# Kernel tuning notes

Hardware: AMD Instinct MI355X
Metric: run time of the kernel (lower is better)

The kernel has to match this reference:

```python
import jax, jax.numpy as jnp
import numpy as np

# ---- static config (matches module defaults / init_kwargs) ----
SX = 256; SY = 256; C = 3; NK = 12; B = 4
R = 10; DT = 0.2; DD = 5; SIGMA = 0.65; THETA_A = 1.0; N_EXP = 2


def _build_kernels():
    """Replicates compute_kernel(): multi-ring Lenia kernels, normalized in real space."""
    rng = np.random.default_rng(42)
    mid = SX // 2
    g = np.mgrid[-mid:mid, -mid:mid]
    dist = np.linalg.norm(g, axis=0)  # [SX, SY]
    Ks = []
    for _ in range(NK):
        r = rng.uniform(0.3, 1.0)
        a = rng.uniform(0.0, 1.0, 3)
        w = rng.uniform(0.05, 0.2, 3)
        b = rng.uniform(0.0, 1.0, 3)
        D = dist / ((R + 15) * r)
        sig = 1.0 / (1.0 + np.exp((D - 1.0) * 10.0))  # sigmoid(-(D-1)*10)
        kerf = (b[None, None, :] * np.exp(-(((D[..., None] - a[None, None, :]) / w[None, None, :]) ** 2) / 2.0)).sum(-1)
        Ks.append(sig * kerf)
    K = np.stack(Ks, axis=-1)  # [SX, SY, NK]
    Kn = K / K.sum(axis=(0, 1), keepdims=True)
    m = rng.uniform(0.05, 0.5, NK)
    s = rng.uniform(0.01, 0.18, NK)
    h = rng.uniform(0.2, 1.0, NK)
    return (Kn.astype(np.float32), m.astype(np.float32), s.astype(np.float32), h.astype(np.float32))


def setup_inputs() -> dict:
    key = jax.random.key(0)
    Kn, m, s, h = _build_kernels()
    A = jax.random.uniform(key, (B, 1, SX, SY, C), dtype=jnp.float32)
    c0 = jnp.asarray(np.arange(NK) % C, dtype=jnp.int32)      # source channel of each kernel
    c1_map = jnp.asarray(np.arange(NK) % C, dtype=jnp.int32)  # target channel of each kernel
    return {"A": A, "Kn": jnp.asarray(Kn), "m": jnp.asarray(m), "s": jnp.asarray(s),
            "h": jnp.asarray(h), "c0": c0, "c1_map": c1_map}


def _sobel(A):
    """Circular (torus) Sobel, separable [1,2,1]x[-1,0,1]/8, on spatial axes (2,3).
    A: [B,1,SX,SY,C] -> [B,1,SX,SY,2,C] (d/dx, d/dy)."""
    sy = jnp.roll(A, -1, 3) + 2.0 * A + jnp.roll(A, 1, 3)
    gx = (jnp.roll(sy, -1, 2) - jnp.roll(sy, 1, 2)) / 8.0
    sx = jnp.roll(A, -1, 2) + 2.0 * A + jnp.roll(A, 1, 2)
    gy = (jnp.roll(sx, -1, 3) - jnp.roll(sx, 1, 3)) / 8.0
    return jnp.stack([gx, gy], axis=4)


def _forward(A, Kn, m, s, h, c0, c1_map):
    # FFT-domain convolution per kernel
    fK = jnp.fft.fft2(jnp.fft.fftshift(Kn, axes=(0, 1)), axes=(0, 1))  # [SX,SY,NK] complex
    fA = jnp.fft.fft2(A, axes=(2, 3))                                   # [B,1,SX,SY,C]
    fAk = fA[..., c0]                                                    # [B,1,SX,SY,NK]
    U = jnp.fft.ifft2(fK[None, None] * fAk, axes=(2, 3)).real           # [B,1,SX,SY,NK]
    # growth(U,m,s) = 2*bell(U,m,s)-1, scaled by h
    G = (2.0 * jnp.exp(-((U - m) ** 2) / (2.0 * s ** 2)) - 1.0) * h
    # sum kernel contributions into their target channel (c1)
    M = jax.nn.one_hot(c1_map, C, dtype=G.dtype)                         # [NK,C]
    Uc = jnp.einsum('bzxyk,kc->bzxyc', G, M)                             # [B,1,SX,SY,C]
    nabla_U = _sobel(Uc)                                                 # [B,1,SX,SY,2,C]
    nabla_A = _sobel(A.sum(-1, keepdims=True))                           # [B,1,SX,SY,2,1]
    alpha = jnp.clip((A[:, :, :, :, None, :] / THETA_A) ** N_EXP, 0.0, 1.0)
    F = nabla_U * (1.0 - alpha) - nabla_A * alpha                        # flow field
    # ---- reintegration tracking (RT) over a (2*DD+1)^2 neighborhood ----
    x = jnp.arange(SX, dtype=F.dtype); y = jnp.arange(SY, dtype=F.dtype)
    pos = jnp.stack(jnp.meshgrid(x, y, indexing='ij'), axis=-1) + 0.5    # [SX,SY,2]
    ma = DD - SIGMA
    mus = pos[None, None, :, :, :, None] + jnp.clip(DT * F, -ma, ma)     # target centers [B,1,SX,SY,2,C]
    offsets = jnp.asarray([(dx, dy) for dx in range(-DD, DD + 1) for dy in range(-DD, DD + 1)], dtype=jnp.int32)
    amax = min(1.0, 2.0 * SIGMA)

    def body(acc, off):
        dx, dy = off[0], off[1]
        rollA = jnp.roll(A, (dx, dy), axis=(2, 3))
        rollmu = jnp.roll(mus, (dx, dy), axis=(2, 3))
        dpmu = jnp.abs(pos[None, None, :, :, :, None] - rollmu)
        sz = 0.5 - dpmu + SIGMA
        area = jnp.prod(jnp.clip(sz, 0.0, amax), axis=4) / (4.0 * SIGMA ** 2)  # [B,1,SX,SY,C]
        return acc + rollA * area, None

    nA, _ = jax.lax.scan(jax.checkpoint(body), jnp.zeros_like(A), offsets)
    return nA


def reference(A, Kn, m, s, h, c0, c1_map):
    return _forward(A, Kn, m, s, h, c0, c1_map)
```

## Files before the change

kernel.cpp:

```cpp
#include <hip/hip_runtime.h>


typedef _Float16 f16;
typedef __attribute__((ext_vector_type(8))) _Float16 half8;
typedef __attribute__((ext_vector_type(16))) float f32x16;

#define RMAX 44
#define NROWS 89
#define NDMAX 8
#define NFRAG (3*NROWS*NDMAX)
#define ST 168
#define TROWS 120
#define SCHED_STRIDE 1024
#define KTHR 1e-7f

__global__ __launch_bounds__(128) void lenia_meta(const float* __restrict__ Kn,
                                                  int2* __restrict__ meta,
                                                  int* __restrict__ rowr) {
    int blk = blockIdx.x;
    int c = blk / NROWS, ri = blk - c * NROWS;
    int di = ri - RMAX;
    int t = threadIdx.x;
    int dj = t - RMAX;
    int act = 0;
    if (t < NROWS) {
        size_t base = (size_t)(((di + 128) << 8) | (dj + 128)) * 12 + c;
        float k0 = Kn[base], k1 = Kn[base + 3], k2 = Kn[base + 6], k3 = Kn[base + 9];
        act = (fmaxf(fmaxf(k0, k1), fmaxf(k2, k3)) > KTHR) ? 1 : 0;
    }
    __shared__ int smn[128], smx[128];
    smn[t] = act ? dj : 1000;
    smx[t] = act ? dj : -1000;
    __syncthreads();
    for (int s = 64; s > 0; s >>= 1) {
        if (t < s) { smn[t] = min(smn[t], smn[t + s]); smx[t] = max(smx[t], smx[t + s]); }
        __syncthreads();
    }
    if (t == 0) {
        int jmn = smn[0], jmx = smx[0];
        if (jmx < jmn) { meta[blk] = make_int2(1, 0); rowr[blk] = 0; }
        else {
            meta[blk] = make_int2(jmn, jmx);
            rowr[blk] = max(abs(di), max(abs(jmn), abs(jmx)));
        }
    }
}

__global__ __launch_bounds__(128) void lenia_sched(const int2* __restrict__ meta,
                                                   const int* __restrict__ rowr,
                                                   int2* __restrict__ meta2,
                                                   unsigned int* __restrict__ sched,
                                                   int* __restrict__ nsched,
                                                   int* __restrict__ radii) {
    int c = blockIdx.x;
    int t = threadIdx.x;
    __shared__ int pre[NROWS], nds[NROWS], rmx[128];
    int nd = 0, d0 = 0;
    if (t < NROWS) {
        int2 bm = meta[c * NROWS + t];
        if (bm.y >= bm.x) {
            d0 = ((bm.x - 7) >> 3) << 3;
            nd = ((bm.y + 7 - d0) >> 4) + 1;
        }
        meta2[c * NROWS + t] = make_int2(d0, nd);
        nds[t] = nd;
    }
    rmx[t] = (t < NROWS) ? rowr[c * NROWS + t] : 0;
    __syncthreads();
    for (int s = 64; s > 0; s >>= 1) {
        if (t < s) rmx[t] = max(rmx[t], rmx[t + s]);
        __syncthreads();
    }
    __shared__ int tot;
    if (t == 0) {
        radii[c] = rmx[0];
        int acc = 0;
        for (int i = 0; i < NROWS; ++i) { pre[i] = acc; acc += nds[i]; }
        tot = acc;
    }
    __syncthreads();
    if (t < NROWS && nd > 0) {
        int base = pre[t];
        for (int i = 0; i < nd; ++i) {
            int delta = d0 + 16 * i;
            unsigned int off = (unsigned int)(t * ST + delta + 128);
            sched[c * SCHED_STRIDE + base + i] =
                (unsigned int)((c * NROWS + t) * NDMAX + i) | (off << 12);
        }
    }
    if (t == 0) {
        int ns = (tot + 7) & ~7;
        unsigned int padoff = (unsigned int)(RMAX * ST + 128);
        for (int i = tot; i < ns + 48; ++i)
            sched[c * SCHED_STRIDE + i] = (unsigned int)NFRAG | (padoff << 12);
        nsched[c] = ns;
    }
}

__global__ __launch_bounds__(256) void lenia_trans(const float* __restrict__ Kn,
                                                   const float* __restrict__ A,
                                                   f16* __restrict__ Ktr,
                                                   f16* __restrict__ Atr) {
    int blk = blockIdx.x, tid = threadIdx.x;
    if (blk < 256) {
        int gid = blk * 256 + tid;
        const float4* kp = (const float4*)(Kn + (size_t)gid * 12);
        float4 v0 = kp[0], v1 = kp[1], v2 = kp[2];
        Ktr[0 * 65536 + gid]  = (f16)v0.x;  Ktr[1 * 65536 + gid]  = (f16)v0.y;
        Ktr[2 * 65536 + gid]  = (f16)v0.z;  Ktr[3 * 65536 + gid]  = (f16)v0.w;
        Ktr[4 * 65536 + gid]  = (f16)v1.x;  Ktr[5 * 65536 + gid]  = (f16)v1.y;
        Ktr[6 * 65536 + gid]  = (f16)v1.z;  Ktr[7 * 65536 + gid]  = (f16)v1.w;
        Ktr[8 * 65536 + gid]  = (f16)v2.x;  Ktr[9 * 65536 + gid]  = (f16)v2.y;
        Ktr[10 * 65536 + gid] = (f16)v2.z;  Ktr[11 * 65536 + gid] = (f16)v2.w;
    } else {
        int px = (blk - 256) * 256 + tid;
        int b = px >> 16, rem = px & 65535;
        const float* ap = A + (size_t)px * 3;
        Atr[(size_t)(b * 3 + 0) * 65536 + rem] = (f16)ap[0];
        Atr[(size_t)(b * 3 + 1) * 65536 + rem] = (f16)ap[1];
        Atr[(size_t)(b * 3 + 2) * 65536 + rem] = (f16)ap[2];
    }
}

__global__ __launch_bounds__(256) void lenia_bpack(const f16* __restrict__ Ktr,
                                                   const int2* __restrict__ meta2,
                                                   uint4* __restrict__ bpack) {
    int fi = blockIdx.x * 4 + (threadIdx.x >> 6);
    int l = threadIdx.x & 63;
    if (fi > NFRAG) return;
    union { f16 h[8]; uint4 u; } pk;
    if (fi == NFRAG) {
        pk.u = make_uint4(0, 0, 0, 0);
        bpack[(size_t)fi * 64 + l] = pk.u;
        return;
    }
    int c = fi / (NROWS * NDMAX);
    int rem = fi - c * (NROWS * NDMAX);
    int ri = rem >> 3, didx = rem & 7;
    int di = ri - RMAX;
    int delta = meta2[c * NROWS + ri].x + 16 * didx;
    int q = (l & 31) >> 3, sy = l & 7, g = l >> 5;
    int dj0 = delta + 8 * g - sy;
    const f16* src = Ktr + (size_t)(c + 3 * q) * 65536 + ((di + 128) << 8) + (dj0 + 128);
    #pragma unroll
    for (int j = 0; j < 8; ++j) pk.h[j] = src[j];
    bpack[(size_t)fi * 64 + l] = pk.u;
}

__global__ __launch_bounds__(256) void lenia_conv(
        const f16* __restrict__ Atr, const uint4* __restrict__ bpack,
        const unsigned int* __restrict__ sched, const int* __restrict__ nsched,
        const int* __restrict__ radii,
        const float* __restrict__ mp, const float* __restrict__ sp,
        const float* __restrict__ hp, f16* __restrict__ Uc) {
    extern __shared__ f16 smh[];

    const int tid = threadIdx.x;
    const int bc = blockIdx.y;
    const int b = bc / 3, c = bc - b * 3;
    const int x0 = (blockIdx.x >> 3) << 5;
    const int y0 = (blockIdx.x & 7) << 5;

    const int R = __builtin_amdgcn_readfirstlane(min(max(radii[c], 1), RMAX));
    const int R8 = (R + 7) & ~7;
    const int colbase = y0 - R8 - 16;
    const int rows = 32 + 2 * R;
    const f16* Ap = Atr + (size_t)(b * 3 + c) * 65536;

    {
        int nchunk = rows * 21;
        int tr = tid / 21, rem = tid - tr * 21;
        for (int ci = tid; ci < nchunk; ci += 256) {
            int gi = (x0 - R + tr) & 255;
            int gj = (colbase + rem * 8) & 255;
            *(half8*)(smh + tr * ST + rem * 8) = *(const half8*)(Ap + (gi << 8) + gj);
            tr += 12; rem += 4;
            if (rem >= 21) { rem -= 21; ++tr; }
        }
    }
    __syncthreads();

    const int lane = tid & 63, wid = tid >> 6;
    const int m = lane & 31, g = lane >> 5;
    const int abase = (m + R - RMAX) * ST + 8 * wid + R8 + 16 + 8 * g - 128;

    const unsigned int* sW = sched + c * SCHED_STRIDE;
    const int ns = __builtin_amdgcn_readfirstlane(nsched[c]);

    f32x16 accE, accO;
    #pragma unroll
    for (int r = 0; r < 16; ++r) { accE[r] = 0.f; accO[r] = 0.f; }

    unsigned int eq[16];
    uint4 bq[16];
    #pragma unroll
    for (int j = 0; j < 16; ++j) {
        eq[j] = sW[j];
        bq[j] = bpack[(size_t)(eq[j] & 4095u) * 64 + lane];
    }

    for (int it = 0; it < ns; it += 16) {
        #pragma unroll
        for (int j = 0; j < 16; j += 2) {
            {
                half8 av = *(const half8*)(smh + abase + (int)(eq[j] >> 12));
                union { uint4 u; half8 h; } bb; bb.u = bq[j];
                accE = __builtin_amdgcn_mfma_f32_32x32x16_f16(av, bb.h, accE, 0, 0, 0);
                unsigned int ne = sW[it + 16 + j];
                eq[j] = ne;
                bq[j] = bpack[(size_t)(ne & 4095u) * 64 + lane];
            }
            {
                half8 av = *(const half8*)(smh + abase + (int)(eq[j + 1] >> 12));
                union { uint4 u; half8 h; } bb; bb.u = bq[j + 1];
                accO = __builtin_amdgcn_mfma_f32_32x32x16_f16(av, bb.h, accO, 0, 0, 0);
                unsigned int ne = sW[it + 17 + j];
                eq[j + 1] = ne;
                bq[j + 1] = bpack[(size_t)(ne & 4095u) * 64 + lane];
            }
        }
    }

    const int q = (lane & 31) >> 3, sy = lane & 7;
    const float mq = mp[c + 3 * q];
    const float sq = sp[c + 3 * q];
    const float hq = hp[c + 3 * q];
    const float i2s = 1.f / (2.f * sq * sq);
    #pragma unroll
    for (int r = 0; r < 16; ++r) {
        float d = (accE[r] + accO[r]) - mq;
        float gg = (2.f * expf(-d * d * i2s) - 1.f) * hq;
        gg += __shfl_xor(gg, 8);
        gg += __shfl_xor(gg, 16);
        if ((lane & 24) == 0) {
            int row = (r & 3) + ((r >> 2) << 3) + (g << 2);
            Uc[((size_t)(b << 16) + ((x0 + row) << 8) + (y0 + 8 * wid + sy)) * 3 + c] = (f16)gg;
        }
    }
}

#define FTW 44
#define FSW 45
#define PLH (FSW * FTW)
__global__ __launch_bounds__(256) void lenia_flowrt(
        const f16* __restrict__ Atr, const f16* __restrict__ Uc,
        float* __restrict__ out) {
    extern __shared__ char fraw[];
    f16*    ucp = (f16*)fraw;
    f16*    atp = (f16*)(fraw + PLH * 2);
    float2* muq = (float2*)(fraw + 8 * PLH);

    int bc = blockIdx.y;
    int b = bc / 3, c = bc - b * 3;
    int t = blockIdx.x;
    int x0 = (t >> 3) << 5, y0 = (t & 7) << 5;
    const f16* A0 = Atr + (size_t)(b * 3) * 65536;
    const f16* Ub = Uc + ((size_t)b << 16) * 3;

    for (int idx = threadIdx.x; idx < FTW * FTW; idx += 256) {
        int si = idx / FTW, sj = idx - si * FTW;
        int gi = (x0 - 6 + si) & 255, gj = (y0 - 6 + sj) & 255;
        int pix = (gi << 8) + gj;
        int o = si * FSW + sj;
        ucp[o] = Ub[(size_t)pix * 3 + c];
        atp[o] = A0[pix];
        atp[PLH + o] = A0[65536 + pix];
        atp[2 * PLH + o] = A0[131072 + pix];
    }
    __syncthreads();

    for (int idx = threadIdx.x; idx < 42 * 42; idx += 256) {
        int ci = idx / 42, cj = idx - ci * 42;
        int si = ci + 1, sj = cj + 1;
        int o = si * FSW + sj;
        int vx = x0 - 6 + si, vy = y0 - 6 + sj;
        float sx = (vx < 0 || vx > 255) ? 1e7f : 0.f;
        float syv = (vy < 0 || vy > 255) ? 1e7f : 0.f;

        float as[3][3];
        #pragma unroll
        for (int i = 0; i < 3; ++i)
            #pragma unroll
            for (int j = 0; j < 3; ++j) {
                int oo = o + (i - 1) * FSW + (j - 1);
                as[i][j] = (float)atp[oo] + (float)atp[PLH + oo] + (float)atp[2 * PLH + oo];
            }
        float gxA = ((as[2][0] + 2.f * as[2][1] + as[2][2])
                   - (as[0][0] + 2.f * as[0][1] + as[0][2])) * 0.125f;
        float gyA = ((as[0][2] + 2.f * as[1][2] + as[2][2])
                   - (as[0][0] + 2.f * as[1][0] + as[2][0])) * 0.125f;

        float u00 = ucp[o - FSW - 1], u01 = ucp[o - FSW], u02 = ucp[o - FSW + 1];
        float u10 = ucp[o - 1],                          u12 = ucp[o + 1];
        float u20 = ucp[o + FSW - 1], u21 = ucp[o + FSW], u22 = ucp[o + FSW + 1];
        float gx = ((u20 + 2.f * u21 + u22) - (u00 + 2.f * u01 + u02)) * 0.125f;
        float gy = ((u02 + 2.f * u12 + u22) - (u00 + 2.f * u10 + u20)) * 0.125f;
        float a = (float)atp[c * PLH + o];
        float alpha = fminf(a * a, 1.f);
        float Fx = gx * (1.f - alpha) - gxA * alpha;
        float Fy = gy * (1.f - alpha) - gyA * alpha;
        float dx = fminf(fmaxf(0.2f * Fx, -4.35f), 4.35f) + sx;
        float dy = fminf(fmaxf(0.2f * Fy, -4.35f), 4.35f) + syv;
        muq[o] = make_float2(dx, dy);
    }
    __syncthreads();

    int tx = threadIdx.x & 31, tyg = threadIdx.x >> 5;
    int ty0 = tyg << 2;
    float a0 = 0.f, a1 = 0.f, a2 = 0.f, a3 = 0.f;
    const f16* ac = atp + c * PLH;

    for (int dxs = 0; dxs < 11; ++dxs) {
        float fdx = (float)(5 - dxs);
        int rowb = (tx + 1 + dxs) * FSW + (ty0 + 1);
        #pragma unroll
        for (int sjj = 0; sjj < 14; ++sjj) {
            float fdy = (float)(5 - sjj);
            float2 mu = muq[rowb + sjj];
            float av = (float)ac[rowb + sjj];
            float wx = fminf(fmaxf(1.15f - fabsf(fdx - mu.x), 0.f), 1.f);
            float awx = av * wx;
            float e0 = fdy - mu.y;
            a0 = fmaf(awx, fminf(fmaxf(1.15f - fabsf(e0), 0.f), 1.f), a0);
            a1 = fmaf(awx, fminf(fmaxf(1.15f - fabsf(e0 + 1.f), 0.f), 1.f), a1);
            a2 = fmaf(awx, fminf(fmaxf(1.15f - fabsf(e0 + 2.f), 0.f), 1.f), a2);
            a3 = fmaf(awx, fminf(fmaxf(1.15f - fabsf(e0 + 3.f), 0.f), 1.f), a3);
        }
    }
    const float inv = 1.0f / 1.69f;
    size_t ob = ((size_t)(b << 16) + ((x0 + tx) << 8) + (y0 + ty0)) * 3 + c;
    out[ob]     = a0 * inv;
    out[ob + 3] = a1 * inv;
    out[ob + 6] = a2 * inv;
    out[ob + 9] = a3 * inv;
}

extern "C" void kernel_launch(void* const* d_in, const int* in_sizes, int n_in,
                              void* d_out, int out_size, void* d_ws, size_t ws_size,
                              hipStream_t stream) {
    const float* A  = (const float*)d_in[0];
    const float* Kn = (const float*)d_in[1];
    const float* m  = (const float*)d_in[2];
    const float* s  = (const float*)d_in[3];
    const float* h  = (const float*)d_in[4];

    char* ws = (char*)d_ws;
    int*          radii = (int*)ws;
    int*          nschd = (int*)(ws + 16);
    int*          rowr  = (int*)(ws + 64);
    int2*         meta  = (int2*)(ws + 2048);
    int2*         meta2 = (int2*)(ws + 8192);
    unsigned int* sched = (unsigned int*)(ws + 16384);
    f16*          Ktr   = (f16*)(ws + 32768);
    f16*          Atr   = (f16*)(ws + 1605632);
    uint4*        bpack = (uint4*)(ws + 3178496);
    f16*          Uc    = (f16*)(ws + 32768);

    lenia_meta<<<3 * NROWS, 128, 0, stream>>>(Kn, meta, rowr);
    lenia_sched<<<3, 128, 0, stream>>>(meta, rowr, meta2, sched, nschd, radii);
    lenia_trans<<<1280, 256, 0, stream>>>(Kn, A, Ktr, Atr);
    lenia_bpack<<<(NFRAG + 4) / 4, 256, 0, stream>>>(Ktr, meta2, bpack);
    lenia_conv<<<dim3(64, 12), 256, TROWS * ST * sizeof(f16), stream>>>(
        Atr, bpack, sched, nschd, radii, m, s, h, Uc);
    lenia_flowrt<<<dim3(64, 12), 256, 8 * PLH + PLH * 8, stream>>>(
        Atr, Uc, (float*)d_out);
}
```

Measured before the change: 74.95 us.

## Fuse kernel transpose into bpack and scalarize schedule loads in conv

Removes the separate Ktr fp16 transpose of the full kernel tensor and builds the MFMA B-fragments straight from Kn inside a merged prep kernel that also converts A. This drops one launch and a full write and read of the 1.5 MB transposed kernel buffer, at the cost of strided 12-float reads from Kn when packing. The conv loop also wraps schedule entries in readfirstlane so the offsets stay uniform scalars, which can cut VGPR use and vector address math. The workspace layout is reassigned so Uc no longer aliases the removed Ktr region.

```diff
diff --git a/kernel.cpp b/kernel.cpp
--- a/kernel.cpp
+++ b/kernel.cpp
@@ -9,6 +9,7 @@
 #define NROWS 89
 #define NDMAX 8
 #define NFRAG (3*NROWS*NDMAX)
+#define NBPK ((NFRAG + 4) / 4)
 #define ST 168
 #define TROWS 120
 #define SCHED_STRIDE 1024
@@ -97,54 +98,41 @@
     }
 }
 
-__global__ __launch_bounds__(256) void lenia_trans(const float* __restrict__ Kn,
+__global__ __launch_bounds__(256) void lenia_prep2(const float* __restrict__ Kn,
                                                    const float* __restrict__ A,
-                                                   f16* __restrict__ Ktr,
+                                                   const int2* __restrict__ meta2,
+                                                   uint4* __restrict__ bpack,
                                                    f16* __restrict__ Atr) {
-    int blk = blockIdx.x, tid = threadIdx.x;
-    if (blk < 256) {
-        int gid = blk * 256 + tid;
-        const float4* kp = (const float4*)(Kn + (size_t)gid * 12);
-        float4 v0 = kp[0], v1 = kp[1], v2 = kp[2];
-        Ktr[0 * 65536 + gid]  = (f16)v0.x;  Ktr[1 * 65536 + gid]  = (f16)v0.y;
-        Ktr[2 * 65536 + gid]  = (f16)v0.z;  Ktr[3 * 65536 + gid]  = (f16)v0.w;
-        Ktr[4 * 65536 + gid]  = (f16)v1.x;  Ktr[5 * 65536 + gid]  = (f16)v1.y;
-        Ktr[6 * 65536 + gid]  = (f16)v1.z;  Ktr[7 * 65536 + gid]  = (f16)v1.w;
-        Ktr[8 * 65536 + gid]  = (f16)v2.x;  Ktr[9 * 65536 + gid]  = (f16)v2.y;
-        Ktr[10 * 65536 + gid] = (f16)v2.z;  Ktr[11 * 65536 + gid] = (f16)v2.w;
+    int blk = blockIdx.x;
+    if (blk < NBPK) {
+        int fi = blk * 4 + (threadIdx.x >> 6);
+        int l = threadIdx.x & 63;
+        if (fi > NFRAG) return;
+        union { f16 h[8]; uint4 u; } pk;
+        if (fi == NFRAG) {
+            pk.u = make_uint4(0, 0, 0, 0);
+            bpack[(size_t)fi * 64 + l] = pk.u;
+            return;
+        }
+        int c = fi / (NROWS * NDMAX);
+        int rem = fi - c * (NROWS * NDMAX);
+        int ri = rem >> 3, didx = rem & 7;
+        int di = ri - RMAX;
+        int delta = meta2[c * NROWS + ri].x + 16 * didx;
+        int q = (l & 31) >> 3, sy = l & 7, g = l >> 5;
+        int dj0 = delta + 8 * g - sy;
+        const float* src = Kn + (size_t)(((di + 128) << 8) + (dj0 + 128)) * 12 + c + 3 * q;
+        #pragma unroll
+        for (int j = 0; j < 8; ++j) pk.h[j] = (f16)src[j * 12];
+        bpack[(size_t)fi * 64 + l] = pk.u;
     } else {
-        int px = (blk - 256) * 256 + tid;
+        int px = (blk - NBPK) * 256 + threadIdx.x;
         int b = px >> 16, rem = px & 65535;
         const float* ap = A + (size_t)px * 3;
         Atr[(size_t)(b * 3 + 0) * 65536 + rem] = (f16)ap[0];
         Atr[(size_t)(b * 3 + 1) * 65536 + rem] = (f16)ap[1];
         Atr[(size_t)(b * 3 + 2) * 65536 + rem] = (f16)ap[2];
     }
-}
-
-__global__ __launch_bounds__(256) void lenia_bpack(const f16* __restrict__ Ktr,
-                                                   const int2* __restrict__ meta2,
-                                                   uint4* __restrict__ bpack) {
-    int fi = blockIdx.x * 4 + (threadIdx.x >> 6);
-    int l = threadIdx.x & 63;
-    if (fi > NFRAG) return;
-    union { f16 h[8]; uint4 u; } pk;
-    if (fi == NFRAG) {
-        pk.u = make_uint4(0, 0, 0, 0);
-        bpack[(size_t)fi * 64 + l] = pk.u;
-        return;
-    }
-    int c = fi / (NROWS * NDMAX);
-    int rem = fi - c * (NROWS * NDMAX);
-    int ri = rem >> 3, didx = rem & 7;
-    int di = ri - RMAX;
-    int delta = meta2[c * NROWS + ri].x + 16 * didx;
-    int q = (l & 31) >> 3, sy = l & 7, g = l >> 5;
-    int dj0 = delta + 8 * g - sy;
-    const f16* src = Ktr + (size_t)(c + 3 * q) * 65536 + ((di + 128) << 8) + (dj0 + 128);
-    #pragma unroll
-    for (int j = 0; j < 8; ++j) pk.h[j] = src[j];
-    bpack[(size_t)fi * 64 + l] = pk.u;
 }
 
 __global__ __launch_bounds__(256) void lenia_conv(
@@ -191,32 +179,33 @@
     #pragma unroll
     for (int r = 0; r < 16; ++r) { accE[r] = 0.f; accO[r] = 0.f; }
 
-    unsigned int eq[16];
+    int eq[16];
     uint4 bq[16];
     #pragma unroll
     for (int j = 0; j < 16; ++j) {
-        eq[j] = sW[j];
-        bq[j] = bpack[(size_t)(eq[j] & 4095u) * 64 + lane];
+        int e = __builtin_amdgcn_readfirstlane((int)sW[j]);
+        eq[j] = e;
+        bq[j] = bpack[(size_t)(e & 4095) * 64 + lane];
     }
 
     for (int it = 0; it < ns; it += 16) {
         #pragma unroll
         for (int j = 0; j < 16; j += 2) {
             {
-                half8 av = *(const half8*)(smh + abase + (int)(eq[j] >> 12));
+                half8 av = *(const half8*)(smh + abase + (eq[j] >> 12));
                 union { uint4 u; half8 h; } bb; bb.u = bq[j];
                 accE = __builtin_amdgcn_mfma_f32_32x32x16_f16(av, bb.h, accE, 0, 0, 0);
-                unsigned int ne = sW[it + 16 + j];
+                int ne = __builtin_amdgcn_readfirstlane((int)sW[it + 16 + j]);
                 eq[j] = ne;
-                bq[j] = bpack[(size_t)(ne & 4095u) * 64 + lane];
+                bq[j] = bpack[(size_t)(ne & 4095) * 64 + lane];
             }
             {
-                half8 av = *(const half8*)(smh + abase + (int)(eq[j + 1] >> 12));
+                half8 av = *(const half8*)(smh + abase + (eq[j + 1] >> 12));
                 union { uint4 u; half8 h; } bb; bb.u = bq[j + 1];
                 accO = __builtin_amdgcn_mfma_f32_32x32x16_f16(av, bb.h, accO, 0, 0, 0);
-                unsigned int ne = sW[it + 17 + j];
+                int ne = __builtin_amdgcn_readfirstlane((int)sW[it + 17 + j]);
                 eq[j + 1] = ne;
-                bq[j + 1] = bpack[(size_t)(ne & 4095u) * 64 + lane];
+                bq[j + 1] = bpack[(size_t)(ne & 4095) * 64 + lane];
             }
         }
     }
@@ -351,15 +340,13 @@
     int2*         meta  = (int2*)(ws + 2048);
     int2*         meta2 = (int2*)(ws + 8192);
     unsigned int* sched = (unsigned int*)(ws + 16384);
-    f16*          Ktr   = (f16*)(ws + 32768);
-    f16*          Atr   = (f16*)(ws + 1605632);
-    uint4*        bpack = (uint4*)(ws + 3178496);
-    f16*          Uc    = (f16*)(ws + 32768);
+    f16*          Atr   = (f16*)(ws + 32768);
+    uint4*        bpack = (uint4*)(ws + 1605632);
+    f16*          Uc    = (f16*)(ws + 3793920);
 
     lenia_meta<<<3 * NROWS, 128, 0, stream>>>(Kn, meta, rowr);
     lenia_sched<<<3, 128, 0, stream>>>(meta, rowr, meta2, sched, nschd, radii);
-    lenia_trans<<<1280, 256, 0, stream>>>(Kn, A, Ktr, Atr);
-    lenia_bpack<<<(NFRAG + 4) / 4, 256, 0, stream>>>(Ktr, meta2, bpack);
+    lenia_prep2<<<NBPK + 1024, 256, 0, stream>>>(Kn, A, meta2, bpack, Atr);
     lenia_conv<<<dim3(64, 12), 256, TROWS * ST * sizeof(f16), stream>>>(
         Atr, bpack, sched, nschd, radii, m, s, h, Uc);
     lenia_flowrt<<<dim3(64, 12), 256, 8 * PLH + PLH * 8, stream>>>(
```

After: 74.67 us. Within noise of the previous version (-0.4%).
